# Kernel tuning notes

Measured on AMD Instinct MI355X. Metric: run time of the kernel, lower is better.

Reference implementation:

```python
import jax, jax.numpy as jnp
import numpy as np
from jax import lax

CHUNK = 128
DECAY_SCALE = 1.0


def setup_inputs() -> dict:
    key = jax.random.key(0)
    k1, k2, k3, k4 = jax.random.split(key, 4)
    Bsz, H, S, dh, ds = 4, 16, 4096, 64, 128
    X = jax.random.normal(k1, (Bsz, H, S, dh), dtype=jnp.float32)
    # log-decay values in (-1, 0) so exp(cumsum) is a stable decay
    A = -jax.random.uniform(k2, (Bsz, H, S), dtype=jnp.float32)
    B_mat = jax.random.normal(k3, (Bsz, H, S, ds), dtype=jnp.float32)
    C = jax.random.normal(k4, (Bsz, H, S, ds), dtype=jnp.float32)
    h0 = jnp.zeros((Bsz, H, ds, dh), dtype=jnp.float32)
    return {"X": X, "A": A, "B_mat": B_mat, "C": C, "h0": h0}


def _ssd_scan(X, A, B_mat, C, h0):
    Bsz, H, S, dh = X.shape
    ds = B_mat.shape[-1]
    cs = CHUNK
    nc = S // cs
    causal = jnp.tril(jnp.ones((cs, cs), dtype=bool))  # [cs, cs]

    # reshape to chunks and put chunk index first for lax.scan
    def to_chunks(t):
        t = t.reshape(Bsz, H, nc, cs, *t.shape[3:])
        return jnp.moveaxis(t, 2, 0)  # [nc, B, H, cs, ...]

    Xc_all = to_chunks(X)
    Ac_all = to_chunks(A)
    Bc_all = to_chunks(B_mat)
    Cc_all = to_chunks(C)

    def step(h_prev, inputs):
        Xc, Ac, Bc, Cc = inputs  # [B,H,cs,dh], [B,H,cs], [B,H,cs,ds] x2
        A_cumsum = jnp.cumsum(Ac * DECAY_SCALE, axis=-1)  # [B,H,cs]
        # causal decay matrix L[i,j] = exp(cumsum_i - cumsum_j) for i>=j
        diff = A_cumsum[..., :, None] - A_cumsum[..., None, :]
        L = jnp.where(causal, jnp.exp(diff), 0.0)  # [B,H,cs,cs]
        CB = jnp.einsum('bhid,bhjd->bhij', Cc, Bc)
        Y_intra = jnp.einsum('bhij,bhjd->bhid', L * CB, Xc)
        decay_from_start = jnp.exp(A_cumsum)  # [B,H,cs]
        Y_inter = jnp.einsum('bhis,bhsd,bhi->bhid', Cc, h_prev, decay_from_start)
        decay_to_end = jnp.exp(A_cumsum[:, :, -1:] - A_cumsum)  # [B,H,cs]
        h_contrib = jnp.einsum('bhts,bhtd,bht->bhsd', Bc, Xc, decay_to_end)
        decay_total = jnp.exp(A_cumsum[:, :, -1])  # [B,H]
        h_end = decay_total[:, :, None, None] * h_prev + h_contrib
        return h_end, Y_intra + Y_inter

    h_final, Y_chunks = lax.scan(step, h0, (Xc_all, Ac_all, Bc_all, Cc_all))
    # Y_chunks: [nc, B, H, cs, dh] -> [B, H, S, dh]
    Y = jnp.moveaxis(Y_chunks, 0, 2).reshape(Bsz, H, S, dh)
    return Y, h_final


def reference(X, A, B_mat, C, h0):
    return _ssd_scan(X, A, B_mat, C, h0)
```

## Files before the change

### kernel.cpp

```cpp
#include <hip/hip_runtime.h>

#define CS 128
#define DH 64
#define DS 128
#define NC 32
#define NBH 64
#define SEQ 4096

typedef __attribute__((ext_vector_type(8))) short short8;
typedef __attribute__((ext_vector_type(4))) short short4v;
typedef __attribute__((ext_vector_type(4))) float f32x4;

__device__ __forceinline__ void bsplit(float x, short &h, short &l) {
  unsigned u = __float_as_uint(x);
  h = (short)(unsigned short)(u >> 16);
  float r = x - __uint_as_float(u & 0xffff0000u);
  l = (short)(unsigned short)(__float_as_uint(r) >> 16);
}

__device__ __forceinline__ void split4(float4 v, short4v &h, short4v &l) {
  short h0,h1,h2,h3,l0,l1,l2,l3;
  bsplit(v.x,h0,l0); bsplit(v.y,h1,l1); bsplit(v.z,h2,l2); bsplit(v.w,h3,l3);
  h = (short4v){h0,h1,h2,h3};
  l = (short4v){l0,l1,l2,l3};
}

__global__ __launch_bounds__(256, 4) void p1_hcontrib(
    const float* __restrict__ A, const float* __restrict__ X,
    const float* __restrict__ B, float* __restrict__ hbuf,
    float* __restrict__ dtot)
{
  __shared__ float csum[CS];
  __shared__ float Xs[32][65];
  __shared__ float Bs[32][129];

  const int blk = blockIdx.x;
  const int bh  = blk >> 5;
  const int c   = blk & 31;
  const int tid = threadIdx.x;
  const int lane = tid & 63, w = tid >> 6;
  const int g4 = lane >> 4, l15 = lane & 15;

  const float* Ac = A + bh * SEQ + c * CS;
  const float* Xc = X + (size_t)(bh * SEQ + c * CS) * DH;
  const float* Bc = B + (size_t)(bh * SEQ + c * CS) * DS;
  float* hout = hbuf + (size_t)blk * DS * DH;

  if (tid < CS) csum[tid] = Ac[tid];
  __syncthreads();
  for (int off = 1; off < CS; off <<= 1) {
    float v = 0.f;
    if (tid < CS) { v = csum[tid]; if (tid >= off) v += csum[tid - off]; }
    __syncthreads();
    if (tid < CS) csum[tid] = v;
    __syncthreads();
  }
  const float cl = csum[CS - 1];
  if (tid == 0) dtot[blk] = __expf(cl);

  f32x4 acc[4][2];
#pragma unroll
  for (int mt = 0; mt < 4; ++mt)
#pragma unroll
    for (int n = 0; n < 2; ++n) acc[mt][n] = (f32x4){0.f,0.f,0.f,0.f};

  for (int kt = 0; kt < 4; ++kt) {
    const int t0 = kt * 32;
#pragma unroll
    for (int m = 0; m < 2; ++m) {
      int q = m * 256 + tid; int r = q >> 4, c4 = q & 15;
      float4 v = *(const float4*)(Xc + (size_t)(t0 + r) * DH + c4 * 4);
      Xs[r][c4*4+0] = v.x; Xs[r][c4*4+1] = v.y; Xs[r][c4*4+2] = v.z; Xs[r][c4*4+3] = v.w;
    }
#pragma unroll
    for (int m = 0; m < 4; ++m) {
      int q = m * 256 + tid; int r = q >> 5, c4 = q & 31;
      float4 v = *(const float4*)(Bc + (size_t)(t0 + r) * DS + c4 * 4);
      Bs[r][c4*4+0] = v.x; Bs[r][c4*4+1] = v.y; Bs[r][c4*4+2] = v.z; Bs[r][c4*4+3] = v.w;
    }
    __syncthreads();

    float dte[8];
#pragma unroll
    for (int j = 0; j < 8; ++j) dte[j] = __expf(cl - csum[t0 + g4 * 8 + j]);

    short8 xh[4], xl[4];
#pragma unroll
    for (int mt = 0; mt < 4; ++mt)
#pragma unroll
      for (int j = 0; j < 8; ++j) {
        short h, l; bsplit(Xs[g4 * 8 + j][mt * 16 + l15], h, l);
        xh[mt][j] = h; xl[mt][j] = l;
      }
#pragma unroll
    for (int ntl = 0; ntl < 2; ++ntl) {
      const int scol = w * 32 + ntl * 16 + l15;
      short8 bh8, bl8;
#pragma unroll
      for (int j = 0; j < 8; ++j) {
        short h, l; bsplit(Bs[g4 * 8 + j][scol] * dte[j], h, l);
        bh8[j] = h; bl8[j] = l;
      }
#pragma unroll
      for (int mt = 0; mt < 4; ++mt) {
        acc[mt][ntl] = __builtin_amdgcn_mfma_f32_16x16x32_bf16(xh[mt], bh8, acc[mt][ntl], 0, 0, 0);
        acc[mt][ntl] = __builtin_amdgcn_mfma_f32_16x16x32_bf16(xh[mt], bl8, acc[mt][ntl], 0, 0, 0);
        acc[mt][ntl] = __builtin_amdgcn_mfma_f32_16x16x32_bf16(xl[mt], bh8, acc[mt][ntl], 0, 0, 0);
      }
    }
    __syncthreads();
  }
#pragma unroll
  for (int mt = 0; mt < 4; ++mt)
#pragma unroll
    for (int ntl = 0; ntl < 2; ++ntl)
#pragma unroll
      for (int r = 0; r < 4; ++r)
        hout[(size_t)(mt * 16 + g4 * 4 + r) * DS + w * 32 + ntl * 16 + l15] = acc[mt][ntl][r];
}

__global__ __launch_bounds__(256) void p2_scan(
    const float* __restrict__ h0, const float* __restrict__ dtot,
    float* __restrict__ hbuf, float* __restrict__ hfinal)
{
  int g = blockIdx.x * 256 + threadIdx.x;
  int bh = g >> 13;
  int e  = g & 8191;
  int d  = e >> 7, sidx = e & 127;
  size_t h0i = (size_t)bh * 8192 + sidx * 64 + d;
  float s = h0[h0i];
  const float* dt = dtot + bh * NC;
  float* p = hbuf + (size_t)bh * NC * 8192 + e;
#pragma unroll 1
  for (int cc = 0; cc < NC; ++cc) {
    float hc = p[(size_t)cc * 8192];
    p[(size_t)cc * 8192] = s;
    s = fmaf(dt[cc], s, hc);
  }
  hfinal[h0i] = s;
}

__global__ __launch_bounds__(256, 3) void p3_y(
    const float* __restrict__ A, const float* __restrict__ X,
    const float* __restrict__ B, const float* __restrict__ C,
    const float* __restrict__ hbuf, float* __restrict__ Y)
{
  __shared__ float csum[CS];
  __shared__ __align__(16) char smem[51200];

  short* Chi = (short*)smem;
  short* Clo = Chi + 5120;
  short* Bhi = Clo + 5120;
  short* Blo = Bhi + 5120;
  short* Hhi = Blo + 5120;
  short* Hlo = Hhi + 2560;
  short* Thi = (short*)smem;
  short* Tlo = Thi + 5120;
  float* Xs  = (float*)(smem + 20480);

  const int blk = blockIdx.x;
  const int bh  = blk >> 5;
  const int c   = blk & 31;
  const int tid = threadIdx.x;
  const int lane = tid & 63, w = tid >> 6;
  const int g4 = lane >> 4, l15 = lane & 15;
  const int w32 = w * 32;

  const float* Ac = A + bh * SEQ + c * CS;
  const float* Xc = X + (size_t)(bh * SEQ + c * CS) * DH;
  const float* Bc = B + (size_t)(bh * SEQ + c * CS) * DS;
  const float* Cc = C + (size_t)(bh * SEQ + c * CS) * DS;
  const float* hst = hbuf + (size_t)blk * DS * DH;
  float* Yc = Y + (size_t)(bh * SEQ + c * CS) * DH;

  if (tid < CS) csum[tid] = Ac[tid];
  __syncthreads();
  for (int off = 1; off < CS; off <<= 1) {
    float v = 0.f;
    if (tid < CS) { v = csum[tid]; if (tid >= off) v += csum[tid - off]; }
    __syncthreads();
    if (tid < CS) csum[tid] = v;
    __syncthreads();
  }

  float csI[2][4];
#pragma unroll
  for (int mt = 0; mt < 2; ++mt)
#pragma unroll
    for (int r = 0; r < 4; ++r) csI[mt][r] = csum[w32 + mt * 16 + g4 * 4 + r];

  f32x4 accCB[2][8];
  f32x4 accY[2][4];
#pragma unroll
  for (int mt = 0; mt < 2; ++mt) {
#pragma unroll
    for (int n = 0; n < 8; ++n) accCB[mt][n] = (f32x4){0.f,0.f,0.f,0.f};
#pragma unroll
    for (int n = 0; n < 4; ++n) accY[mt][n] = (f32x4){0.f,0.f,0.f,0.f};
  }

  for (int kt = 0; kt < 4; ++kt) {
    const int k0 = kt * 32;
#pragma unroll
    for (int m = 0; m < 4; ++m) {
      int q = m * 256 + tid; int r = q >> 3, c4 = q & 7;
      short4v hv, lv;
      float4 v = *(const float4*)(Cc + (size_t)r * DS + k0 + c4 * 4);
      split4(v, hv, lv);
      *(short4v*)(Chi + r * 40 + c4 * 4) = hv;
      *(short4v*)(Clo + r * 40 + c4 * 4) = lv;
      float4 vb = *(const float4*)(Bc + (size_t)r * DS + k0 + c4 * 4);
      split4(vb, hv, lv);
      *(short4v*)(Bhi + r * 40 + c4 * 4) = hv;
      *(short4v*)(Blo + r * 40 + c4 * 4) = lv;
    }
#pragma unroll
    for (int m = 0; m < 2; ++m) {
      int q = m * 256 + tid; int r = q >> 3, c4 = q & 7;
      short4v hv, lv;
      float4 v = *(const float4*)(hst + (size_t)r * DS + k0 + c4 * 4);
      split4(v, hv, lv);
      *(short4v*)(Hhi + r * 40 + c4 * 4) = hv;
      *(short4v*)(Hlo + r * 40 + c4 * 4) = lv;
    }
    __syncthreads();

    short8 ah[2], al[2];
#pragma unroll
    for (int mt = 0; mt < 2; ++mt) {
      ah[mt] = *(const short8*)(Chi + (w32 + mt * 16 + l15) * 40 + g4 * 8);
      al[mt] = *(const short8*)(Clo + (w32 + mt * 16 + l15) * 40 + g4 * 8);
    }
#pragma unroll
    for (int nt = 0; nt < 8; ++nt) {
      short8 bh8 = *(const short8*)(Bhi + (nt * 16 + l15) * 40 + g4 * 8);
      short8 bl8 = *(const short8*)(Blo + (nt * 16 + l15) * 40 + g4 * 8);
#pragma unroll
      for (int mt = 0; mt < 2; ++mt) {
        accCB[mt][nt] = __builtin_amdgcn_mfma_f32_16x16x32_bf16(ah[mt], bh8, accCB[mt][nt], 0, 0, 0);
        accCB[mt][nt] = __builtin_amdgcn_mfma_f32_16x16x32_bf16(ah[mt], bl8, accCB[mt][nt], 0, 0, 0);
        accCB[mt][nt] = __builtin_amdgcn_mfma_f32_16x16x32_bf16(al[mt], bh8, accCB[mt][nt], 0, 0, 0);
      }
    }
#pragma unroll
    for (int nd = 0; nd < 4; ++nd) {
      short8 hh = *(const short8*)(Hhi + (nd * 16 + l15) * 40 + g4 * 8);
      short8 hl = *(const short8*)(Hlo + (nd * 16 + l15) * 40 + g4 * 8);
#pragma unroll
      for (int mt = 0; mt < 2; ++mt) {
        accY[mt][nd] = __builtin_amdgcn_mfma_f32_16x16x32_bf16(ah[mt], hh, accY[mt][nd], 0, 0, 0);
        accY[mt][nd] = __builtin_amdgcn_mfma_f32_16x16x32_bf16(ah[mt], hl, accY[mt][nd], 0, 0, 0);
        accY[mt][nd] = __builtin_amdgcn_mfma_f32_16x16x32_bf16(al[mt], hh, accY[mt][nd], 0, 0, 0);
      }
    }
    __syncthreads();
  }

#pragma unroll
  for (int mt = 0; mt < 2; ++mt)
#pragma unroll
    for (int r = 0; r < 4; ++r) {
      float ei = __expf(csI[mt][r]);
#pragma unroll
      for (int nd = 0; nd < 4; ++nd) accY[mt][nd][r] *= ei;
    }

#pragma unroll
  for (int jt = 0; jt < 4; ++jt) {
#pragma unroll
    for (int ntb = 0; ntb < 2; ++ntb) {
      const int nt = jt * 2 + ntb;
      const int jj = ntb * 16 + l15;
      const int j  = jt * 32 + jj;
      const float csj = csum[j];
#pragma unroll
      for (int mt = 0; mt < 2; ++mt)
#pragma unroll
        for (int r = 0; r < 4; ++r) {
          int i = w32 + mt * 16 + g4 * 4 + r;
          float v = (i >= j) ? accCB[mt][nt][r] * __expf(csI[mt][r] - csj) : 0.f;
          short h, l; bsplit(v, h, l);
          Thi[i * 40 + jj] = h;
          Tlo[i * 40 + jj] = l;
        }
    }
#pragma unroll
    for (int m = 0; m < 2; ++m) {
      int q = m * 256 + tid; int r = q >> 4, c4 = q & 15;
      float4 v = *(const float4*)(Xc + (size_t)(jt * 32 + r) * DH + c4 * 4);
      Xs[r * 65 + c4*4+0] = v.x; Xs[r * 65 + c4*4+1] = v.y;
      Xs[r * 65 + c4*4+2] = v.z; Xs[r * 65 + c4*4+3] = v.w;
    }
    __syncthreads();

    short8 th[2], tl[2];
#pragma unroll
    for (int mt = 0; mt < 2; ++mt) {
      th[mt] = *(const short8*)(Thi + (w32 + mt * 16 + l15) * 40 + g4 * 8);
      tl[mt] = *(const short8*)(Tlo + (w32 + mt * 16 + l15) * 40 + g4 * 8);
    }
#pragma unroll
    for (int nd = 0; nd < 4; ++nd) {
      short8 xh8, xl8;
#pragma unroll
      for (int jq = 0; jq < 8; ++jq) {
        short h, l; bsplit(Xs[(g4 * 8 + jq) * 65 + nd * 16 + l15], h, l);
        xh8[jq] = h; xl8[jq] = l;
      }
#pragma unroll
      for (int mt = 0; mt < 2; ++mt) {
        accY[mt][nd] = __builtin_amdgcn_mfma_f32_16x16x32_bf16(th[mt], xh8, accY[mt][nd], 0, 0, 0);
        accY[mt][nd] = __builtin_amdgcn_mfma_f32_16x16x32_bf16(th[mt], xl8, accY[mt][nd], 0, 0, 0);
        accY[mt][nd] = __builtin_amdgcn_mfma_f32_16x16x32_bf16(tl[mt], xh8, accY[mt][nd], 0, 0, 0);
      }
    }
    __syncthreads();
  }

#pragma unroll
  for (int mt = 0; mt < 2; ++mt)
#pragma unroll
    for (int nd = 0; nd < 4; ++nd)
#pragma unroll
      for (int r = 0; r < 4; ++r)
        Yc[(size_t)(w32 + mt * 16 + g4 * 4 + r) * DH + nd * 16 + l15] = accY[mt][nd][r];
}

extern "C" void kernel_launch(void* const* d_in, const int* in_sizes, int n_in,
                              void* d_out, int out_size, void* d_ws, size_t ws_size,
                              hipStream_t stream)
{
  const float* X  = (const float*)d_in[0];
  const float* A  = (const float*)d_in[1];
  const float* B  = (const float*)d_in[2];
  const float* C  = (const float*)d_in[3];
  const float* h0 = (const float*)d_in[4];

  float* Y      = (float*)d_out;
  float* hfinal = Y + (size_t)NBH * SEQ * DH;

  float* hbuf = (float*)d_ws;
  float* dtot = hbuf + (size_t)NBH * NC * DS * DH;

  dim3 blk(256);
  p1_hcontrib<<<dim3(NBH * NC), blk, 0, stream>>>(A, X, B, hbuf, dtot);
  p2_scan<<<dim3((NBH * DS * DH) / 256), blk, 0, stream>>>(h0, dtot, hbuf, hfinal);
  p3_y<<<dim3(NBH * NC), blk, 0, stream>>>(A, X, B, C, hbuf, Y);
}
```

Before: 474.8 us.

## Load MFMA fragments directly from global and use wave-shuffle cumsum scans

Both the h-contribution and output kernels drop their shared-memory staging of X, B, C and the chunk state. Each lane now loads its MFMA fragments straight from global memory and splits them into bf16 hi/lo pairs in registers. The block-wide shared-memory prefix sum over the decay values becomes a per-wave shuffle scan, which removes many __syncthreads barriers and most LDS usage. In exchange, waves issue redundant and less coalesced global loads: every wave reloads all of B, and X is read element-wise with a stride. Performance then depends on L1/L2 hit rates rather than on LDS reuse.

```diff
diff --git a/kernel.cpp b/kernel.cpp
--- a/kernel.cpp
+++ b/kernel.cpp
@@ -8,7 +8,6 @@
 #define SEQ 4096
 
 typedef __attribute__((ext_vector_type(8))) short short8;
-typedef __attribute__((ext_vector_type(4))) short short4v;
 typedef __attribute__((ext_vector_type(4))) float f32x4;
 
 __device__ __forceinline__ void bsplit(float x, short &h, short &l) {
@@ -18,11 +17,16 @@
   l = (short)(unsigned short)(__float_as_uint(r) >> 16);
 }
 
-__device__ __forceinline__ void split4(float4 v, short4v &h, short4v &l) {
-  short h0,h1,h2,h3,l0,l1,l2,l3;
-  bsplit(v.x,h0,l0); bsplit(v.y,h1,l1); bsplit(v.z,h2,l2); bsplit(v.w,h3,l3);
-  h = (short4v){h0,h1,h2,h3};
-  l = (short4v){l0,l1,l2,l3};
+__device__ __forceinline__ void split8(const float4 v0, const float4 v1, short8 &h, short8 &l) {
+  short hh, ll;
+  bsplit(v0.x,hh,ll); h[0]=hh; l[0]=ll;
+  bsplit(v0.y,hh,ll); h[1]=hh; l[1]=ll;
+  bsplit(v0.z,hh,ll); h[2]=hh; l[2]=ll;
+  bsplit(v0.w,hh,ll); h[3]=hh; l[3]=ll;
+  bsplit(v1.x,hh,ll); h[4]=hh; l[4]=ll;
+  bsplit(v1.y,hh,ll); h[5]=hh; l[5]=ll;
+  bsplit(v1.z,hh,ll); h[6]=hh; l[6]=ll;
+  bsplit(v1.w,hh,ll); h[7]=hh; l[7]=ll;
 }
 
 __global__ __launch_bounds__(256, 4) void p1_hcontrib(
@@ -30,32 +34,28 @@
     const float* __restrict__ B, float* __restrict__ hbuf,
     float* __restrict__ dtot)
 {
-  __shared__ float csum[CS];
-  __shared__ float Xs[32][65];
-  __shared__ float Bs[32][129];
-
   const int blk = blockIdx.x;
   const int bh  = blk >> 5;
   const int c   = blk & 31;
   const int tid = threadIdx.x;
   const int lane = tid & 63, w = tid >> 6;
   const int g4 = lane >> 4, l15 = lane & 15;
+  const int w32 = w * 32;
 
   const float* Ac = A + bh * SEQ + c * CS;
   const float* Xc = X + (size_t)(bh * SEQ + c * CS) * DH;
   const float* Bc = B + (size_t)(bh * SEQ + c * CS) * DS;
   float* hout = hbuf + (size_t)blk * DS * DH;
 
-  if (tid < CS) csum[tid] = Ac[tid];
-  __syncthreads();
-  for (int off = 1; off < CS; off <<= 1) {
-    float v = 0.f;
-    if (tid < CS) { v = csum[tid]; if (tid >= off) v += csum[tid - off]; }
-    __syncthreads();
-    if (tid < CS) csum[tid] = v;
-    __syncthreads();
-  }
-  const float cl = csum[CS - 1];
+  float a0 = Ac[lane], a1 = Ac[64 + lane];
+#pragma unroll
+  for (int off = 1; off < 64; off <<= 1) {
+    float t0 = __shfl_up(a0, off, 64);
+    float t1 = __shfl_up(a1, off, 64);
+    if (lane >= off) { a0 += t0; a1 += t1; }
+  }
+  a1 += __shfl(a0, 63, 64);
+  const float cl = __shfl(a1, 63, 64);
   if (tid == 0) dtot[blk] = __expf(cl);
 
   f32x4 acc[4][2];
@@ -64,41 +64,33 @@
 #pragma unroll
     for (int n = 0; n < 2; ++n) acc[mt][n] = (f32x4){0.f,0.f,0.f,0.f};
 
+#pragma unroll 1
   for (int kt = 0; kt < 4; ++kt) {
     const int t0 = kt * 32;
-#pragma unroll
-    for (int m = 0; m < 2; ++m) {
-      int q = m * 256 + tid; int r = q >> 4, c4 = q & 15;
-      float4 v = *(const float4*)(Xc + (size_t)(t0 + r) * DH + c4 * 4);
-      Xs[r][c4*4+0] = v.x; Xs[r][c4*4+1] = v.y; Xs[r][c4*4+2] = v.z; Xs[r][c4*4+3] = v.w;
-    }
-#pragma unroll
-    for (int m = 0; m < 4; ++m) {
-      int q = m * 256 + tid; int r = q >> 5, c4 = q & 31;
-      float4 v = *(const float4*)(Bc + (size_t)(t0 + r) * DS + c4 * 4);
-      Bs[r][c4*4+0] = v.x; Bs[r][c4*4+1] = v.y; Bs[r][c4*4+2] = v.z; Bs[r][c4*4+3] = v.w;
-    }
-    __syncthreads();
-
     float dte[8];
 #pragma unroll
-    for (int j = 0; j < 8; ++j) dte[j] = __expf(cl - csum[t0 + g4 * 8 + j]);
-
+    for (int j = 0; j < 8; ++j) {
+      int p = t0 + g4 * 8 + j;
+      float cs = __shfl(kt < 2 ? a0 : a1, p & 63, 64);
+      dte[j] = __expf(cl - cs);
+    }
     short8 xh[4], xl[4];
 #pragma unroll
     for (int mt = 0; mt < 4; ++mt)
 #pragma unroll
       for (int j = 0; j < 8; ++j) {
-        short h, l; bsplit(Xs[g4 * 8 + j][mt * 16 + l15], h, l);
+        float x = Xc[(size_t)(t0 + g4 * 8 + j) * DH + mt * 16 + l15];
+        short h, l; bsplit(x, h, l);
         xh[mt][j] = h; xl[mt][j] = l;
       }
 #pragma unroll
     for (int ntl = 0; ntl < 2; ++ntl) {
-      const int scol = w * 32 + ntl * 16 + l15;
+      const int scol = w32 + ntl * 16 + l15;
       short8 bh8, bl8;
 #pragma unroll
       for (int j = 0; j < 8; ++j) {
-        short h, l; bsplit(Bs[g4 * 8 + j][scol] * dte[j], h, l);
+        float bv = Bc[(size_t)(t0 + g4 * 8 + j) * DS + scol] * dte[j];
+        short h, l; bsplit(bv, h, l);
         bh8[j] = h; bl8[j] = l;
       }
 #pragma unroll
@@ -108,7 +100,6 @@
         acc[mt][ntl] = __builtin_amdgcn_mfma_f32_16x16x32_bf16(xl[mt], bh8, acc[mt][ntl], 0, 0, 0);
       }
     }
-    __syncthreads();
   }
 #pragma unroll
   for (int mt = 0; mt < 4; ++mt)
@@ -116,7 +107,7 @@
     for (int ntl = 0; ntl < 2; ++ntl)
 #pragma unroll
       for (int r = 0; r < 4; ++r)
-        hout[(size_t)(mt * 16 + g4 * 4 + r) * DS + w * 32 + ntl * 16 + l15] = acc[mt][ntl][r];
+        hout[(size_t)(mt * 16 + g4 * 4 + r) * DS + w32 + ntl * 16 + l15] = acc[mt][ntl][r];
 }
 
 __global__ __launch_bounds__(256) void p2_scan(
@@ -145,18 +136,8 @@
     const float* __restrict__ B, const float* __restrict__ C,
     const float* __restrict__ hbuf, float* __restrict__ Y)
 {
-  __shared__ float csum[CS];
-  __shared__ __align__(16) char smem[51200];
-
-  short* Chi = (short*)smem;
-  short* Clo = Chi + 5120;
-  short* Bhi = Clo + 5120;
-  short* Blo = Bhi + 5120;
-  short* Hhi = Blo + 5120;
-  short* Hlo = Hhi + 2560;
-  short* Thi = (short*)smem;
-  short* Tlo = Thi + 5120;
-  float* Xs  = (float*)(smem + 20480);
+  __shared__ short Thi[128 * 40];
+  __shared__ short Tlo[128 * 40];
 
   const int blk = blockIdx.x;
   const int bh  = blk >> 5;
@@ -173,21 +154,14 @@
   const float* hst = hbuf + (size_t)blk * DS * DH;
   float* Yc = Y + (size_t)(bh * SEQ + c * CS) * DH;
 
-  if (tid < CS) csum[tid] = Ac[tid];
-  __syncthreads();
-  for (int off = 1; off < CS; off <<= 1) {
-    float v = 0.f;
-    if (tid < CS) { v = csum[tid]; if (tid >= off) v += csum[tid - off]; }
-    __syncthreads();
-    if (tid < CS) csum[tid] = v;
-    __syncthreads();
-  }
-
-  float csI[2][4];
-#pragma unroll
-  for (int mt = 0; mt < 2; ++mt)
-#pragma unroll
-    for (int r = 0; r < 4; ++r) csI[mt][r] = csum[w32 + mt * 16 + g4 * 4 + r];
+  float a0 = Ac[lane], a1 = Ac[64 + lane];
+#pragma unroll
+  for (int off = 1; off < 64; off <<= 1) {
+    float t0 = __shfl_up(a0, off, 64);
+    float t1 = __shfl_up(a1, off, 64);
+    if (lane >= off) { a0 += t0; a1 += t1; }
+  }
+  a1 += __shfl(a0, 63, 64);
 
   f32x4 accCB[2][8];
   f32x4 accY[2][4];
@@ -199,42 +173,20 @@
     for (int n = 0; n < 4; ++n) accY[mt][n] = (f32x4){0.f,0.f,0.f,0.f};
   }
 
+#pragma unroll 1
   for (int kt = 0; kt < 4; ++kt) {
-    const int k0 = kt * 32;
-#pragma unroll
-    for (int m = 0; m < 4; ++m) {
-      int q = m * 256 + tid; int r = q >> 3, c4 = q & 7;
-      short4v hv, lv;
-      float4 v = *(const float4*)(Cc + (size_t)r * DS + k0 + c4 * 4);
-      split4(v, hv, lv);
-      *(short4v*)(Chi + r * 40 + c4 * 4) = hv;
-      *(short4v*)(Clo + r * 40 + c4 * 4) = lv;
-      float4 vb = *(const float4*)(Bc + (size_t)r * DS + k0 + c4 * 4);
-      split4(vb, hv, lv);
-      *(short4v*)(Bhi + r * 40 + c4 * 4) = hv;
-      *(short4v*)(Blo + r * 40 + c4 * 4) = lv;
-    }
-#pragma unroll
-    for (int m = 0; m < 2; ++m) {
-      int q = m * 256 + tid; int r = q >> 3, c4 = q & 7;
-      short4v hv, lv;
-      float4 v = *(const float4*)(hst + (size_t)r * DS + k0 + c4 * 4);
-      split4(v, hv, lv);
-      *(short4v*)(Hhi + r * 40 + c4 * 4) = hv;
-      *(short4v*)(Hlo + r * 40 + c4 * 4) = lv;
-    }
-    __syncthreads();
-
+    const int k0 = kt * 32 + g4 * 8;
     short8 ah[2], al[2];
 #pragma unroll
     for (int mt = 0; mt < 2; ++mt) {
-      ah[mt] = *(const short8*)(Chi + (w32 + mt * 16 + l15) * 40 + g4 * 8);
-      al[mt] = *(const short8*)(Clo + (w32 + mt * 16 + l15) * 40 + g4 * 8);
+      const float* cp = Cc + (size_t)(w32 + mt * 16 + l15) * DS + k0;
+      split8(*(const float4*)cp, *(const float4*)(cp + 4), ah[mt], al[mt]);
     }
 #pragma unroll
     for (int nt = 0; nt < 8; ++nt) {
-      short8 bh8 = *(const short8*)(Bhi + (nt * 16 + l15) * 40 + g4 * 8);
-      short8 bl8 = *(const short8*)(Blo + (nt * 16 + l15) * 40 + g4 * 8);
+      const float* bp = Bc + (size_t)(nt * 16 + l15) * DS + k0;
+      short8 bh8, bl8;
+      split8(*(const float4*)bp, *(const float4*)(bp + 4), bh8, bl8);
 #pragma unroll
       for (int mt = 0; mt < 2; ++mt) {
         accCB[mt][nt] = __builtin_amdgcn_mfma_f32_16x16x32_bf16(ah[mt], bh8, accCB[mt][nt], 0, 0, 0);
@@ -244,18 +196,28 @@
     }
 #pragma unroll
     for (int nd = 0; nd < 4; ++nd) {
-      short8 hh = *(const short8*)(Hhi + (nd * 16 + l15) * 40 + g4 * 8);
-      short8 hl = *(const short8*)(Hlo + (nd * 16 + l15) * 40 + g4 * 8);
+      const float* hp = hst + (size_t)(nd * 16 + l15) * DS + k0;
+      short8 hh8, hl8;
+      split8(*(const float4*)hp, *(const float4*)(hp + 4), hh8, hl8);
 #pragma unroll
       for (int mt = 0; mt < 2; ++mt) {
-        accY[mt][nd] = __builtin_amdgcn_mfma_f32_16x16x32_bf16(ah[mt], hh, accY[mt][nd], 0, 0, 0);
-        accY[mt][nd] = __builtin_amdgcn_mfma_f32_16x16x32_bf16(ah[mt], hl, accY[mt][nd], 0, 0, 0);
-        accY[mt][nd] = __builtin_amdgcn_mfma_f32_16x16x32_bf16(al[mt], hh, accY[mt][nd], 0, 0, 0);
-      }
-    }
-    __syncthreads();
-  }
-
+        accY[mt][nd] = __builtin_amdgcn_mfma_f32_16x16x32_bf16(ah[mt], hh8, accY[mt][nd], 0, 0, 0);
+        accY[mt][nd] = __builtin_amdgcn_mfma_f32_16x16x32_bf16(ah[mt], hl8, accY[mt][nd], 0, 0, 0);
+        accY[mt][nd] = __builtin_amdgcn_mfma_f32_16x16x32_bf16(al[mt], hh8, accY[mt][nd], 0, 0, 0);
+      }
+    }
+  }
+
+  float csI[2][4];
+#pragma unroll
+  for (int mt = 0; mt < 2; ++mt) {
+    const float src = (w32 + mt * 16) < 64 ? a0 : a1;
+#pragma unroll
+    for (int r = 0; r < 4; ++r) {
+      int p = w32 + mt * 16 + g4 * 4 + r;
+      csI[mt][r] = __shfl(src, p & 63, 64);
+    }
+  }
 #pragma unroll
   for (int mt = 0; mt < 2; ++mt)
 #pragma unroll
@@ -272,7 +234,7 @@
       const int nt = jt * 2 + ntb;
       const int jj = ntb * 16 + l15;
       const int j  = jt * 32 + jj;
-      const float csj = csum[j];
+      const float csj = __shfl(jt < 2 ? a0 : a1, j & 63, 64);
 #pragma unroll
       for (int mt = 0; mt < 2; ++mt)
 #pragma unroll
@@ -284,15 +246,6 @@
           Tlo[i * 40 + jj] = l;
         }
     }
-#pragma unroll
-    for (int m = 0; m < 2; ++m) {
-      int q = m * 256 + tid; int r = q >> 4, c4 = q & 15;
-      float4 v = *(const float4*)(Xc + (size_t)(jt * 32 + r) * DH + c4 * 4);
-      Xs[r * 65 + c4*4+0] = v.x; Xs[r * 65 + c4*4+1] = v.y;
-      Xs[r * 65 + c4*4+2] = v.z; Xs[r * 65 + c4*4+3] = v.w;
-    }
-    __syncthreads();
-
     short8 th[2], tl[2];
 #pragma unroll
     for (int mt = 0; mt < 2; ++mt) {
@@ -304,7 +257,8 @@
       short8 xh8, xl8;
 #pragma unroll
       for (int jq = 0; jq < 8; ++jq) {
-        short h, l; bsplit(Xs[(g4 * 8 + jq) * 65 + nd * 16 + l15], h, l);
+        float x = Xc[(size_t)(jt * 32 + g4 * 8 + jq) * DH + nd * 16 + l15];
+        short h, l; bsplit(x, h, l);
         xh8[jq] = h; xl8[jq] = l;
       }
 #pragma unroll
@@ -314,7 +268,6 @@
         accY[mt][nd] = __builtin_amdgcn_mfma_f32_16x16x32_bf16(tl[mt], xh8, accY[mt][nd], 0, 0, 0);
       }
     }
-    __syncthreads();
   }
 
 #pragma unroll
```

Measured after the change: 573.2 us. 1.21x slower.
